# Kernel tuning notes

Hardware: AMD Instinct MI355X
Metric: run time of the kernel (lower is better)

## Reference

```python
import jax, jax.numpy as jnp
import numpy as np

N = 50000      # nodes
E = 800000     # edges (before self-loops)
IN = 128       # in_channels
HID = 32       # hidden_channels
H = 4          # num_heads
OUT = 2        # out_channels
NEG_SLOPE = 0.2


def setup_inputs() -> dict:
    key = jax.random.key(0)
    ks = jax.random.split(key, 16)
    s = 0.1
    x = jax.random.normal(ks[0], (N, IN), jnp.float32)
    edge_index = jax.random.randint(ks[1], (2, E), 0, N, dtype=jnp.int32)
    W1 = jax.random.normal(ks[2], (IN, H * HID), jnp.float32) * s
    att_src1 = jax.random.normal(ks[3], (H, HID), jnp.float32) * s
    att_dst1 = jax.random.normal(ks[4], (H, HID), jnp.float32) * s
    b1 = jnp.zeros((H * HID,), jnp.float32)
    W2 = jax.random.normal(ks[5], (H * HID, H * HID), jnp.float32) * s
    att_src2 = jax.random.normal(ks[6], (H, HID), jnp.float32) * s
    att_dst2 = jax.random.normal(ks[7], (H, HID), jnp.float32) * s
    b2 = jnp.zeros((H * HID,), jnp.float32)
    W3 = jax.random.normal(ks[8], (H * HID, OUT), jnp.float32) * s
    att_src3 = jax.random.normal(ks[9], (1, OUT), jnp.float32) * s
    att_dst3 = jax.random.normal(ks[10], (1, OUT), jnp.float32) * s
    b3 = jnp.zeros((OUT,), jnp.float32)
    return {"x": x, "edge_index": edge_index,
            "W1": W1, "att_src1": att_src1, "att_dst1": att_dst1, "b1": b1,
            "W2": W2, "att_src2": att_src2, "att_dst2": att_dst2, "b2": b2,
            "W3": W3, "att_src3": att_src3, "att_dst3": att_dst3, "b3": b3}


def gat_layer(x, src, dst, W, a_src, a_dst, b, heads, ch, concat):
    """PyG GATConv (eval mode): per-edge LeakyReLU attention, edge-softmax over
    incoming edges of each destination node, weighted scatter-add aggregation."""
    n = x.shape[0]
    h = (x @ W).reshape(n, heads, ch)                      # [N,H,C]
    alpha_s = jnp.sum(h * a_src, axis=-1)                  # [N,H]
    alpha_d = jnp.sum(h * a_dst, axis=-1)                  # [N,H]
    alpha = jax.nn.leaky_relu(alpha_s[src] + alpha_d[dst], NEG_SLOPE)  # [E',H]
    amax = jax.ops.segment_max(alpha, dst, num_segments=n)             # [N,H]
    e = jnp.exp(alpha - amax[dst])
    denom = jax.ops.segment_sum(e, dst, num_segments=n)
    w = e / denom[dst]                                     # softmax weights [E',H]
    out = jax.ops.segment_sum(h[src] * w[:, :, None], dst, num_segments=n)  # [N,H,C]
    out = out.reshape(n, heads * ch) if concat else out.mean(axis=1)
    return out + b


def reference(x, edge_index, W1, att_src1, att_dst1, b1,
              W2, att_src2, att_dst2, b2, W3, att_src3, att_dst3, b3):
    # PyG GATConv adds self-loops by default
    loop = jnp.arange(N, dtype=edge_index.dtype)
    src = jnp.concatenate([edge_index[0], loop])
    dst = jnp.concatenate([edge_index[1], loop])
    h = jax.nn.elu(gat_layer(x, src, dst, W1, att_src1, att_dst1, b1, H, HID, True))
    h = jax.nn.elu(gat_layer(h, src, dst, W2, att_src2, att_dst2, b2, H, HID, True))
    h = gat_layer(h, src, dst, W3, att_src3, att_dst3, b3, 1, OUT, False)
    return jax.nn.log_softmax(h, axis=1)
```

## Files before the change

### kernel.cpp

```cpp
#include <hip/hip_runtime.h>
#include <hip/hip_fp16.h>

#define NN 50000
#define EE 800000
#define ET 850000
#define NEG 0.2f
#define SCAN_B 1024
#define NBLK ((NN + SCAN_B - 1) / SCAN_B)

__device__ __forceinline__ float leaky(float x) { return fmaxf(x, NEG * x); }
__device__ __forceinline__ float elu_f(float x) { return x > 0.f ? x : expm1f(x); }

struct alignas(8) half4 { __half2 a, b; };

typedef _Float16 half8_t __attribute__((ext_vector_type(8)));
typedef float float4_t __attribute__((ext_vector_type(4)));

__global__ void hist_k(const int* __restrict__ ei, int* __restrict__ counts,
                       int* __restrict__ rank) {
    int i = blockIdx.x * blockDim.x + threadIdx.x;
    if (i >= ET) return;
    int dst = (i < EE) ? ei[EE + i] : (i - EE);
    rank[i] = atomicAdd(&counts[dst], 1);
}

__global__ void scan1_k(const int* __restrict__ counts, int* __restrict__ rp,
                        int* __restrict__ bsums) {
    __shared__ int lsum[256];
    int base = blockIdx.x * SCAN_B;
    int v[4];
    int tsum = 0;
#pragma unroll
    for (int j = 0; j < 4; ++j) {
        int i = base + threadIdx.x * 4 + j;
        v[j] = (i < NN) ? counts[i] : 0;
        tsum += v[j];
    }
    lsum[threadIdx.x] = tsum;
    __syncthreads();
    for (int off = 1; off < 256; off <<= 1) {
        int t = (threadIdx.x >= off) ? lsum[threadIdx.x - off] : 0;
        __syncthreads();
        lsum[threadIdx.x] += t;
        __syncthreads();
    }
    int excl = lsum[threadIdx.x] - tsum;
#pragma unroll
    for (int j = 0; j < 4; ++j) {
        int i = base + threadIdx.x * 4 + j;
        if (i < NN) rp[i] = excl;
        excl += v[j];
    }
    if (threadIdx.x == 255) bsums[blockIdx.x] = lsum[255];
}

__global__ void scan2_k(int* __restrict__ bsums, int* __restrict__ rp) {
    int lane = threadIdx.x;
    int v = (lane < NBLK) ? bsums[lane] : 0;
    int orig = v;
    for (int off = 1; off < 64; off <<= 1) {
        int t = __shfl_up(v, off, 64);
        if (lane >= off) v += t;
    }
    if (lane < NBLK) bsums[lane] = v - orig;
    if (lane == 63) rp[NN] = v;
}

__global__ void scan3_k(int* __restrict__ rp, const int* __restrict__ bsums) {
    int add = bsums[blockIdx.x];
    int base = blockIdx.x * SCAN_B + threadIdx.x * 4;
#pragma unroll
    for (int j = 0; j < 4; ++j) {
        int i = base + j;
        if (i < NN) rp[i] += add;
    }
}

__global__ void scatter_k(const int* __restrict__ ei, const int* __restrict__ rp,
                          const int* __restrict__ rank, int* __restrict__ csr) {
    int i = blockIdx.x * blockDim.x + threadIdx.x;
    if (i >= ET) return;
    int src, dst;
    if (i < EE) { src = ei[i]; dst = ei[EE + i]; }
    else        { src = dst = i - EE; }
    csr[rp[dst] + rank[i]] = src;
}

__global__ void wt_k(const float* __restrict__ W, __half* __restrict__ Wt) {
    int i = blockIdx.x * 256 + threadIdx.x;
    int k = i >> 7, n = i & 127;
    Wt[n * 128 + k] = __float2half(W[i]);
}

__global__ __launch_bounds__(256)
void gemm_mfma_k(const float* __restrict__ Xf, const __half* __restrict__ Xh,
                 const __half* __restrict__ Wt, __half* __restrict__ Yh, int nrows,
                 const float* __restrict__ att_s, const float* __restrict__ att_d,
                 float* __restrict__ asb, float* __restrict__ adb) {
    int lane = threadIdx.x & 63;
    int wid  = threadIdx.x >> 6;
    int n = lane & 15, quad = lane >> 4;
    float atts_r[8], attd_r[8];
#pragma unroll
    for (int t = 0; t < 8; ++t) {
        atts_r[t] = att_s[t * 16 + n];
        attd_r[t] = att_d[t * 16 + n];
    }
    for (int row0 = (blockIdx.x * 4 + wid) * 16; row0 < nrows; row0 += gridDim.x * 64) {
        float4_t acc[8];
#pragma unroll
        for (int t = 0; t < 8; ++t) acc[t] = (float4_t){0.f, 0.f, 0.f, 0.f};
        int rA = row0 + n; if (rA >= nrows) rA = nrows - 1;
#pragma unroll
        for (int ch = 0; ch < 4; ++ch) {
            half8_t a;
            if (Xh) {
                a = *(const half8_t*)(Xh + (size_t)rA * 128 + ch * 32 + quad * 8);
            } else {
                const float* xp = Xf + (size_t)rA * 128 + ch * 32 + quad * 8;
                float4 f0 = *(const float4*)xp;
                float4 f1 = *(const float4*)(xp + 4);
                a = (half8_t){(_Float16)f0.x, (_Float16)f0.y, (_Float16)f0.z, (_Float16)f0.w,
                              (_Float16)f1.x, (_Float16)f1.y, (_Float16)f1.z, (_Float16)f1.w};
            }
#pragma unroll
            for (int t = 0; t < 8; ++t) {
                half8_t b = *(const half8_t*)(Wt + (t * 16 + n) * 128 + ch * 32 + quad * 8);
                acc[t] = __builtin_amdgcn_mfma_f32_16x16x32_f16(a, b, acc[t], 0, 0, 0);
            }
        }
#pragma unroll
        for (int rg = 0; rg < 4; ++rg) {
            int row = row0 + quad * 4 + rg;
            if (row < nrows) {
                __half* yp = Yh + (size_t)row * 128 + n;
#pragma unroll
                for (int t = 0; t < 8; ++t)
                    yp[t * 16] = __float2half(acc[t][rg]);
            }
        }
#pragma unroll
        for (int rg = 0; rg < 4; ++rg) {
            float ps[4], pd[4];
#pragma unroll
            for (int h = 0; h < 4; ++h) {
                ps[h] = acc[2*h][rg] * atts_r[2*h] + acc[2*h+1][rg] * atts_r[2*h+1];
                pd[h] = acc[2*h][rg] * attd_r[2*h] + acc[2*h+1][rg] * attd_r[2*h+1];
#pragma unroll
                for (int mask = 1; mask < 16; mask <<= 1) {
                    ps[h] += __shfl_xor(ps[h], mask, 64);
                    pd[h] += __shfl_xor(pd[h], mask, 64);
                }
            }
            int row = row0 + quad * 4 + rg;
            if (n == 0 && row < nrows) {
#pragma unroll
                for (int h = 0; h < 4; ++h) {
                    asb[row * 4 + h] = ps[h];
                    adb[row * 4 + h] = pd[h];
                }
            }
        }
    }
}

__global__ __launch_bounds__(256)
void agg_k(const __half* __restrict__ Hh, const float* __restrict__ asb,
           const float* __restrict__ adb, const int* __restrict__ rp,
           const int* __restrict__ csr, const float* __restrict__ bias,
           __half* __restrict__ Y,
           const float* __restrict__ W3, const float* __restrict__ s3w,
           const float* __restrict__ d3w, float* __restrict__ h3,
           float* __restrict__ as3, float* __restrict__ ad3) {
    int lane = threadIdx.x & 63;
    int hw = lane >> 5;
    int l  = lane & 31;
    int n = blockIdx.x * 8 + (threadIdx.x >> 6) * 2 + hw;
    if (n >= NN) return;
    int hd = l >> 3;
    float ad = adb[n * 4 + hd];
    float acc0 = 0.f, acc1 = 0.f, acc2 = 0.f, acc3 = 0.f, den = 0.f;
    int e = rp[n], end = rp[n + 1], last = end - 1;
    for (int base = e; base < end; base += 8) {
        int s[8]; float a[8]; float2 hraw[8];
#pragma unroll
        for (int j = 0; j < 8; ++j) {
            int i = base + j;
            s[j] = csr[i <= last ? i : last];
        }
#pragma unroll
        for (int j = 0; j < 8; ++j) a[j] = asb[s[j] * 4 + hd] + ad;
#pragma unroll
        for (int j = 0; j < 8; ++j)
            hraw[j] = ((const float2*)(Hh + (size_t)s[j] * 128))[l];
#pragma unroll
        for (int j = 0; j < 8; ++j) {
            float w = __expf(leaky(a[j]));
            w = (base + j <= last) ? w : 0.f;
            den += w;
            const __half2* hp = (const __half2*)&hraw[j];
            float2 f01 = __half22float2(hp[0]);
            float2 f23 = __half22float2(hp[1]);
            acc0 += w * f01.x; acc1 += w * f01.y;
            acc2 += w * f23.x; acc3 += w * f23.y;
        }
    }
    float4 bv = ((const float4*)bias)[l];
    float inv = 1.f / den;
    float o0 = elu_f(acc0 * inv + bv.x);
    float o1 = elu_f(acc1 * inv + bv.y);
    float o2 = elu_f(acc2 * inv + bv.z);
    float o3 = elu_f(acc3 * inv + bv.w);
    if (!W3) {
        half4 hv;
        hv.a = __floats2half2_rn(o0, o1);
        hv.b = __floats2half2_rn(o2, o3);
        ((half4*)(Y + (size_t)n * 128))[l] = hv;
    } else {
        float4 wa = ((const float4*)W3)[l * 2];
        float4 wb = ((const float4*)W3)[l * 2 + 1];
        float p0 = o0 * wa.x + o1 * wa.z + o2 * wb.x + o3 * wb.z;
        float p1 = o0 * wa.y + o1 * wa.w + o2 * wb.y + o3 * wb.w;
        for (int off = 16; off > 0; off >>= 1) {
            p0 += __shfl_down(p0, off, 32);
            p1 += __shfl_down(p1, off, 32);
        }
        if (l == 0) {
            h3[n * 2 + 0] = p0;
            h3[n * 2 + 1] = p1;
            as3[n] = p0 * s3w[0] + p1 * s3w[1];
            ad3[n] = p0 * d3w[0] + p1 * d3w[1];
        }
    }
}

__global__ void l3agg_k(const float* __restrict__ h3, const float* __restrict__ as3,
                        const float* __restrict__ ad3, const int* __restrict__ rp,
                        const int* __restrict__ csr, const float* __restrict__ b3,
                        float* __restrict__ out) {
    int n = blockIdx.x * blockDim.x + threadIdx.x;
    if (n >= NN) return;
    const float2* h2 = (const float2*)h3;
    float adn = ad3[n];
    float den = 0.f, a0 = 0.f, a1 = 0.f;
    int e = rp[n], end = rp[n + 1], last = end - 1;
    for (int base = e; base < end; base += 4) {
        int s[4]; float al[4]; float2 g[4];
#pragma unroll
        for (int j = 0; j < 4; ++j) {
            int i = base + j;
            s[j] = csr[i <= last ? i : last];
        }
#pragma unroll
        for (int j = 0; j < 4; ++j) al[j] = as3[s[j]] + adn;
#pragma unroll
        for (int j = 0; j < 4; ++j) g[j] = h2[s[j]];
#pragma unroll
        for (int j = 0; j < 4; ++j) {
            float w = __expf(leaky(al[j]));
            w = (base + j <= last) ? w : 0.f;
            den += w;
            a0 += w * g[j].x;
            a1 += w * g[j].y;
        }
    }
    float o0 = a0 / den + b3[0];
    float o1 = a1 / den + b3[1];
    float m = fmaxf(o0, o1);
    float lse = m + logf(__expf(o0 - m) + __expf(o1 - m));
    out[n * 2 + 0] = o0 - lse;
    out[n * 2 + 1] = o1 - lse;
}

extern "C" void kernel_launch(void* const* d_in, const int* in_sizes, int n_in,
                              void* d_out, int out_size, void* d_ws, size_t ws_size,
                              hipStream_t stream) {
    const float* x   = (const float*)d_in[0];
    const int*   ei  = (const int*)d_in[1];
    const float* W1  = (const float*)d_in[2];
    const float* as1 = (const float*)d_in[3];
    const float* ad1 = (const float*)d_in[4];
    const float* b1  = (const float*)d_in[5];
    const float* W2  = (const float*)d_in[6];
    const float* as2 = (const float*)d_in[7];
    const float* ad2 = (const float*)d_in[8];
    const float* b2  = (const float*)d_in[9];
    const float* W3  = (const float*)d_in[10];
    const float* s3w = (const float*)d_in[11];
    const float* d3w = (const float*)d_in[12];
    const float* b3  = (const float*)d_in[13];
    float* out = (float*)d_out;

    char* ws = (char*)d_ws;
    size_t off = 0;
    auto alloc = [&](size_t bytes) -> char* {
        char* p = ws + off;
        off = (off + bytes + 255) & ~(size_t)255;
        return p;
    };
    __half* hA    = (__half*)alloc((size_t)NN * 128 * 2);
    __half* hBh   = (__half*)alloc((size_t)NN * 128 * 2);
    float* asb    = (float*)alloc((size_t)NN * 4 * 4);
    float* adb    = (float*)alloc((size_t)NN * 4 * 4);
    int*   rp     = (int*)alloc((size_t)(NN + 1) * 4);
    int*   counts = (int*)alloc((size_t)NN * 4);
    int*   csr    = (int*)alloc((size_t)ET * 4);
    int*   rank   = (int*)alloc((size_t)ET * 4);
    int*   bsums  = (int*)alloc((size_t)NBLK * 4);
    __half* Wt1   = (__half*)alloc(128 * 128 * 2);
    __half* Wt2   = (__half*)alloc(128 * 128 * 2);
    float* h3     = (float*)alloc((size_t)NN * 2 * 4);
    float* s3     = (float*)alloc((size_t)NN * 4);
    float* d3     = (float*)alloc((size_t)NN * 4);

    wt_k<<<64, 256, 0, stream>>>(W1, Wt1);
    wt_k<<<64, 256, 0, stream>>>(W2, Wt2);

    hipMemsetAsync(counts, 0, (size_t)NN * 4, stream);
    hist_k<<<(ET + 255) / 256, 256, 0, stream>>>(ei, counts, rank);
    scan1_k<<<NBLK, 256, 0, stream>>>(counts, rp, bsums);
    scan2_k<<<1, 64, 0, stream>>>(bsums, rp);
    scan3_k<<<NBLK, 256, 0, stream>>>(rp, bsums);
    scatter_k<<<(ET + 255) / 256, 256, 0, stream>>>(ei, rp, rank, csr);

    gemm_mfma_k<<<(NN + 63) / 64, 256, 0, stream>>>(x, nullptr, Wt1, hA, NN,
                                                    as1, ad1, asb, adb);
    agg_k<<<(NN + 7) / 8, 256, 0, stream>>>(hA, asb, adb, rp, csr, b1, hBh,
                                            nullptr, nullptr, nullptr,
                                            nullptr, nullptr, nullptr);

    gemm_mfma_k<<<(NN + 63) / 64, 256, 0, stream>>>(nullptr, hBh, Wt2, hA, NN,
                                                    as2, ad2, asb, adb);
    agg_k<<<(NN + 7) / 8, 256, 0, stream>>>(hA, asb, adb, rp, csr, b2, nullptr,
                                            W3, s3w, d3w, h3, s3, d3);

    l3agg_k<<<(NN + 255) / 256, 256, 0, stream>>>(h3, s3, d3, rp, csr, b3, out);
}
```

Baseline: 288.3 us.

## Overlap layer-1 GEMM with CSR build and fuse small prep/scan kernels

```diff
diff --git a/kernel.cpp b/kernel.cpp
--- a/kernel.cpp
+++ b/kernel.cpp
@@ -7,6 +7,9 @@
 #define NEG 0.2f
 #define SCAN_B 1024
 #define NBLK ((NN + SCAN_B - 1) / SCAN_B)
+#define GHALF 391
+#define RHALF 25024
+#define HIST_BLKS ((ET + 255) / 256)
 
 __device__ __forceinline__ float leaky(float x) { return fmaxf(x, NEG * x); }
 __device__ __forceinline__ float elu_f(float x) { return x > 0.f ? x : expm1f(x); }
@@ -16,12 +19,134 @@
 typedef _Float16 half8_t __attribute__((ext_vector_type(8)));
 typedef float float4_t __attribute__((ext_vector_type(4)));
 
-__global__ void hist_k(const int* __restrict__ ei, int* __restrict__ counts,
-                       int* __restrict__ rank) {
-    int i = blockIdx.x * blockDim.x + threadIdx.x;
-    if (i >= ET) return;
-    int dst = (i < EE) ? ei[EE + i] : (i - EE);
-    rank[i] = atomicAdd(&counts[dst], 1);
+__device__ __forceinline__
+void gemm_tile(const float* __restrict__ Xf, const __half* __restrict__ Xh,
+               const __half* __restrict__ Wt, __half* __restrict__ Yh,
+               int nrows, int row0, int lane,
+               const float* __restrict__ att_s, const float* __restrict__ att_d,
+               float* __restrict__ asb, float* __restrict__ adb) {
+    int n = lane & 15, quad = lane >> 4;
+    float atts_r[8], attd_r[8];
+#pragma unroll
+    for (int t = 0; t < 8; ++t) {
+        atts_r[t] = att_s[t * 16 + n];
+        attd_r[t] = att_d[t * 16 + n];
+    }
+    float4_t acc[8];
+#pragma unroll
+    for (int t = 0; t < 8; ++t) acc[t] = (float4_t){0.f, 0.f, 0.f, 0.f};
+    int rA = row0 + n; if (rA >= nrows) rA = nrows - 1;
+#pragma unroll
+    for (int ch = 0; ch < 4; ++ch) {
+        half8_t a;
+        if (Xh) {
+            a = *(const half8_t*)(Xh + (size_t)rA * 128 + ch * 32 + quad * 8);
+        } else {
+            const float* xp = Xf + (size_t)rA * 128 + ch * 32 + quad * 8;
+            float4 f0 = *(const float4*)xp;
+            float4 f1 = *(const float4*)(xp + 4);
+            a = (half8_t){(_Float16)f0.x, (_Float16)f0.y, (_Float16)f0.z, (_Float16)f0.w,
+                          (_Float16)f1.x, (_Float16)f1.y, (_Float16)f1.z, (_Float16)f1.w};
+        }
+#pragma unroll
+        for (int t = 0; t < 8; ++t) {
+            half8_t b = *(const half8_t*)(Wt + (t * 16 + n) * 128 + ch * 32 + quad * 8);
+            acc[t] = __builtin_amdgcn_mfma_f32_16x16x32_f16(a, b, acc[t], 0, 0, 0);
+        }
+    }
+#pragma unroll
+    for (int rg = 0; rg < 4; ++rg) {
+        int row = row0 + quad * 4 + rg;
+        if (row < nrows) {
+            __half* yp = Yh + (size_t)row * 128 + n;
+#pragma unroll
+            for (int t = 0; t < 8; ++t)
+                yp[t * 16] = __float2half(acc[t][rg]);
+        }
+    }
+#pragma unroll
+    for (int rg = 0; rg < 4; ++rg) {
+        float ps[4], pd[4];
+#pragma unroll
+        for (int h = 0; h < 4; ++h) {
+            ps[h] = acc[2*h][rg] * atts_r[2*h] + acc[2*h+1][rg] * atts_r[2*h+1];
+            pd[h] = acc[2*h][rg] * attd_r[2*h] + acc[2*h+1][rg] * attd_r[2*h+1];
+#pragma unroll
+            for (int mask = 1; mask < 16; mask <<= 1) {
+                ps[h] += __shfl_xor(ps[h], mask, 64);
+                pd[h] += __shfl_xor(pd[h], mask, 64);
+            }
+        }
+        int row = row0 + quad * 4 + rg;
+        if (n == 0 && row < nrows) {
+#pragma unroll
+            for (int h = 0; h < 4; ++h) {
+                asb[row * 4 + h] = ps[h];
+                adb[row * 4 + h] = pd[h];
+            }
+        }
+    }
+}
+
+__global__ __launch_bounds__(256)
+void gemm_mfma_k(const float* __restrict__ Xf, const __half* __restrict__ Xh,
+                 const __half* __restrict__ Wt, __half* __restrict__ Yh, int nrows,
+                 const float* __restrict__ att_s, const float* __restrict__ att_d,
+                 float* __restrict__ asb, float* __restrict__ adb) {
+    int lane = threadIdx.x & 63;
+    int wid  = threadIdx.x >> 6;
+    int row0 = (blockIdx.x * 4 + wid) * 16;
+    if (row0 < nrows)
+        gemm_tile(Xf, Xh, Wt, Yh, nrows, row0, lane, att_s, att_d, asb, adb);
+}
+
+__global__ __launch_bounds__(256)
+void mega_k(const float* __restrict__ Xf, const __half* __restrict__ Wt,
+            __half* __restrict__ Yh, int rowBase,
+            const float* __restrict__ att_s, const float* __restrict__ att_d,
+            float* __restrict__ asb, float* __restrict__ adb,
+            int mode,
+            const int* __restrict__ ei, int* __restrict__ counts,
+            int* __restrict__ rank, const int* __restrict__ rp,
+            int* __restrict__ csr) {
+    int b = blockIdx.x;
+    if (b < GHALF) {
+        int lane = threadIdx.x & 63;
+        int wid  = threadIdx.x >> 6;
+        int row0 = rowBase + (b * 4 + wid) * 16;
+        if (row0 < NN)
+            gemm_tile(Xf, nullptr, Wt, Yh, NN, row0, lane, att_s, att_d, asb, adb);
+    } else {
+        int i = (b - GHALF) * 256 + threadIdx.x;
+        if (i < ET) {
+            if (mode == 0) {
+                int dst = (i < EE) ? ei[EE + i] : (i - EE);
+                rank[i] = atomicAdd(&counts[dst], 1);
+            } else {
+                int src, dst;
+                if (i < EE) { src = ei[i]; dst = ei[EE + i]; }
+                else        { src = dst = i - EE; }
+                csr[rp[dst] + rank[i]] = src;
+            }
+        }
+    }
+}
+
+__global__ void prep_k(const float* __restrict__ W1, __half* __restrict__ Wt1,
+                       const float* __restrict__ W2, __half* __restrict__ Wt2,
+                       int* __restrict__ counts) {
+    int i = blockIdx.x * 256 + threadIdx.x;
+    if (i < 16384) {
+        int k = i >> 7, n = i & 127;
+        Wt1[n * 128 + k] = __float2half(W1[i]);
+    } else if (i < 32768) {
+        int j = i - 16384;
+        int k = j >> 7, n = j & 127;
+        Wt2[n * 128 + k] = __float2half(W2[j]);
+    } else {
+        int j = i - 32768;
+        if (j < NN) counts[j] = 0;
+    }
 }
 
 __global__ void scan1_k(const int* __restrict__ counts, int* __restrict__ rp,
@@ -54,113 +179,28 @@
     if (threadIdx.x == 255) bsums[blockIdx.x] = lsum[255];
 }
 
-__global__ void scan2_k(int* __restrict__ bsums, int* __restrict__ rp) {
-    int lane = threadIdx.x;
-    int v = (lane < NBLK) ? bsums[lane] : 0;
-    int orig = v;
-    for (int off = 1; off < 64; off <<= 1) {
-        int t = __shfl_up(v, off, 64);
-        if (lane >= off) v += t;
-    }
-    if (lane < NBLK) bsums[lane] = v - orig;
-    if (lane == 63) rp[NN] = v;
-}
-
-__global__ void scan3_k(int* __restrict__ rp, const int* __restrict__ bsums) {
-    int add = bsums[blockIdx.x];
-    int base = blockIdx.x * SCAN_B + threadIdx.x * 4;
+__global__ void scan23_k(int* __restrict__ rp, const int* __restrict__ bsums) {
+    __shared__ int sadd;
+    int bx = blockIdx.x;
+    if (threadIdx.x < 64) {
+        int lane = threadIdx.x;
+        int v = (lane < NBLK) ? bsums[lane] : 0;
+        for (int off = 1; off < 64; off <<= 1) {
+            int t = __shfl_up(v, off, 64);
+            if (lane >= off) v += t;
+        }
+        int srcl = (bx == 0) ? 0 : (bx - 1);
+        int ex = __shfl(v, srcl, 64);
+        if (lane == 0) sadd = (bx == 0) ? 0 : ex;
+        if (bx == 0 && lane == 63) rp[NN] = v;
+    }
+    __syncthreads();
+    int add = sadd;
+    int base = bx * SCAN_B + threadIdx.x * 4;
 #pragma unroll
     for (int j = 0; j < 4; ++j) {
         int i = base + j;
         if (i < NN) rp[i] += add;
-    }
-}
-
-__global__ void scatter_k(const int* __restrict__ ei, const int* __restrict__ rp,
-                          const int* __restrict__ rank, int* __restrict__ csr) {
-    int i = blockIdx.x * blockDim.x + threadIdx.x;
-    if (i >= ET) return;
-    int src, dst;
-    if (i < EE) { src = ei[i]; dst = ei[EE + i]; }
-    else        { src = dst = i - EE; }
-    csr[rp[dst] + rank[i]] = src;
-}
-
-__global__ void wt_k(const float* __restrict__ W, __half* __restrict__ Wt) {
-    int i = blockIdx.x * 256 + threadIdx.x;
-    int k = i >> 7, n = i & 127;
-    Wt[n * 128 + k] = __float2half(W[i]);
-}
-
-__global__ __launch_bounds__(256)
-void gemm_mfma_k(const float* __restrict__ Xf, const __half* __restrict__ Xh,
-                 const __half* __restrict__ Wt, __half* __restrict__ Yh, int nrows,
-                 const float* __restrict__ att_s, const float* __restrict__ att_d,
-                 float* __restrict__ asb, float* __restrict__ adb) {
-    int lane = threadIdx.x & 63;
-    int wid  = threadIdx.x >> 6;
-    int n = lane & 15, quad = lane >> 4;
-    float atts_r[8], attd_r[8];
-#pragma unroll
-    for (int t = 0; t < 8; ++t) {
-        atts_r[t] = att_s[t * 16 + n];
-        attd_r[t] = att_d[t * 16 + n];
-    }
-    for (int row0 = (blockIdx.x * 4 + wid) * 16; row0 < nrows; row0 += gridDim.x * 64) {
-        float4_t acc[8];
-#pragma unroll
-        for (int t = 0; t < 8; ++t) acc[t] = (float4_t){0.f, 0.f, 0.f, 0.f};
-        int rA = row0 + n; if (rA >= nrows) rA = nrows - 1;
-#pragma unroll
-        for (int ch = 0; ch < 4; ++ch) {
-            half8_t a;
-            if (Xh) {
-                a = *(const half8_t*)(Xh + (size_t)rA * 128 + ch * 32 + quad * 8);
-            } else {
-                const float* xp = Xf + (size_t)rA * 128 + ch * 32 + quad * 8;
-                float4 f0 = *(const float4*)xp;
-                float4 f1 = *(const float4*)(xp + 4);
-                a = (half8_t){(_Float16)f0.x, (_Float16)f0.y, (_Float16)f0.z, (_Float16)f0.w,
-                              (_Float16)f1.x, (_Float16)f1.y, (_Float16)f1.z, (_Float16)f1.w};
-            }
-#pragma unroll
-            for (int t = 0; t < 8; ++t) {
-                half8_t b = *(const half8_t*)(Wt + (t * 16 + n) * 128 + ch * 32 + quad * 8);
-                acc[t] = __builtin_amdgcn_mfma_f32_16x16x32_f16(a, b, acc[t], 0, 0, 0);
-            }
-        }
-#pragma unroll
-        for (int rg = 0; rg < 4; ++rg) {
-            int row = row0 + quad * 4 + rg;
-            if (row < nrows) {
-                __half* yp = Yh + (size_t)row * 128 + n;
-#pragma unroll
-                for (int t = 0; t < 8; ++t)
-                    yp[t * 16] = __float2half(acc[t][rg]);
-            }
-        }
-#pragma unroll
-        for (int rg = 0; rg < 4; ++rg) {
-            float ps[4], pd[4];
-#pragma unroll
-            for (int h = 0; h < 4; ++h) {
-                ps[h] = acc[2*h][rg] * atts_r[2*h] + acc[2*h+1][rg] * atts_r[2*h+1];
-                pd[h] = acc[2*h][rg] * attd_r[2*h] + acc[2*h+1][rg] * attd_r[2*h+1];
-#pragma unroll
-                for (int mask = 1; mask < 16; mask <<= 1) {
-                    ps[h] += __shfl_xor(ps[h], mask, 64);
-                    pd[h] += __shfl_xor(pd[h], mask, 64);
-                }
-            }
-            int row = row0 + quad * 4 + rg;
-            if (n == 0 && row < nrows) {
-#pragma unroll
-                for (int h = 0; h < 4; ++h) {
-                    asb[row * 4 + h] = ps[h];
-                    adb[row * 4 + h] = pd[h];
-                }
-            }
-        }
     }
 }
 
@@ -313,24 +353,24 @@
     float* s3     = (float*)alloc((size_t)NN * 4);
     float* d3     = (float*)alloc((size_t)NN * 4);
 
-    wt_k<<<64, 256, 0, stream>>>(W1, Wt1);
-    wt_k<<<64, 256, 0, stream>>>(W2, Wt2);
-
-    hipMemsetAsync(counts, 0, (size_t)NN * 4, stream);
-    hist_k<<<(ET + 255) / 256, 256, 0, stream>>>(ei, counts, rank);
+    prep_k<<<(32768 + NN + 255) / 256, 256, 0, stream>>>(W1, Wt1, W2, Wt2, counts);
+
+    mega_k<<<GHALF + HIST_BLKS, 256, 0, stream>>>(x, Wt1, hA, 0, as1, ad1, asb, adb,
+                                                  0, ei, counts, rank, nullptr, nullptr);
+
     scan1_k<<<NBLK, 256, 0, stream>>>(counts, rp, bsums);
-    scan2_k<<<1, 64, 0, stream>>>(bsums, rp);
-    scan3_k<<<NBLK, 256, 0, stream>>>(rp, bsums);
-    scatter_k<<<(ET + 255) / 256, 256, 0, stream>>>(ei, rp, rank, csr);
-
-    gemm_mfma_k<<<(NN + 63) / 64, 256, 0, stream>>>(x, nullptr, Wt1, hA, NN,
-                                                    as1, ad1, asb, adb);
+    scan23_k<<<NBLK, 256, 0, stream>>>(rp, bsums);
+
+    mega_k<<<GHALF + HIST_BLKS, 256, 0, stream>>>(x, Wt1, hA, RHALF, as1, ad1, asb, adb,
+                                                  1, ei, counts, rank, rp, csr);
+
     agg_k<<<(NN + 7) / 8, 256, 0, stream>>>(hA, asb, adb, rp, csr, b1, hBh,
                                             nullptr, nullptr, nullptr,
                                             nullptr, nullptr, nullptr);
 
     gemm_mfma_k<<<(NN + 63) / 64, 256, 0, stream>>>(nullptr, hBh, Wt2, hA, NN,
                                                     as2, ad2, asb, adb);
+
     agg_k<<<(NN + 7) / 8, 256, 0, stream>>>(hA, asb, adb, rp, csr, b2, nullptr,
                                             W3, s3w, d3w, h3, s3, d3);
 
```

Result: faster. 268.3 us (-6.9%).
